# Performance work log

Hardware: AMD Instinct MI355X
Metric: run time of the kernel (lower is better)

## Reference

```python
import jax, jax.numpy as jnp
import numpy as np

B, S, D, R = 8, 512, 1024, 128

def setup_inputs() -> dict:
    key = jax.random.key(0)
    k1, k2 = jax.random.split(key)
    batch = jax.random.normal(k1, (B, S, D), dtype=jnp.float32)
    # nn.init.uniform_(proj, -0.05, 0.05)
    proj = jax.random.uniform(k2, (D, R), dtype=jnp.float32, minval=-0.05, maxval=0.05)
    return {"batch": batch, "proj": proj}

def reference(batch, proj):
    # transformed: [B, S, R]
    transformed = jnp.matmul(batch, proj)
    # pairwise squared distances via broadcast diff (same math as expand/transpose/diff/pow/sum)
    diffs = transformed[:, :, None, :] - transformed[:, None, :, :]  # [B, S, S, R]
    squared_distances = jnp.sum(diffs * diffs, axis=-1)              # [B, S, S]
    return squared_distances
```

## Files before the change

### kernel.cpp

```cpp
#include <hip/hip_runtime.h>
#include <hip/hip_bf16.h>

constexpr int B_ = 8;
constexpr int S_ = 512;
constexpr int D_ = 1024;
constexpr int R_ = 128;
constexpr int M_ = B_ * S_;

typedef unsigned short u16;
typedef __attribute__((ext_vector_type(8))) short short8;
typedef __attribute__((ext_vector_type(4))) float f32x4;

static __device__ __forceinline__ u16 f2bf(float f) {
    unsigned u = __float_as_uint(f);
    u += 0x7fffu + ((u >> 16) & 1u);
    return (u16)(u >> 16);
}
static __device__ __forceinline__ float bf2f(u16 u) {
    return __uint_as_float((unsigned)u << 16);
}

__global__ __launch_bounds__(256) void transpose_proj_kernel(
    const float* __restrict__ P, u16* __restrict__ Pt)
{
    __shared__ float S[16][132];
    const int t  = threadIdx.x;
    const int kk = blockIdx.x;
    const int kq = blockIdx.y;

#pragma unroll
    for (int p = 0; p < 2; ++p) {
        const int k = (t >> 5) + p * 8;
        const int c = (t & 31) * 4;
        *reinterpret_cast<float4*>(&S[k][c]) =
            *reinterpret_cast<const float4*>(
                &P[(size_t)(kk * 64 + kq * 16 + k) * R_ + c]);
    }
    __syncthreads();

    const int col = t >> 1;
    const int h   = t & 1;
    unsigned u[4];
#pragma unroll
    for (int q = 0; q < 4; ++q) {
        const u16 lo = f2bf(S[h * 8 + q * 2 + 0][col]);
        const u16 hi = f2bf(S[h * 8 + q * 2 + 1][col]);
        u[q] = (unsigned)lo | ((unsigned)hi << 16);
    }
    *reinterpret_cast<uint4*>(&Pt[(size_t)kk * 8192 + col * 64 + kq * 16 + h * 8]) =
        make_uint4(u[0], u[1], u[2], u[3]);
}

__global__ __launch_bounds__(256) void gemm1_kernel(
    const float* __restrict__ A,
    const u16* __restrict__ Pt,
    u16* __restrict__ T)
{
    __shared__ u16 As[2][16][72];
    __shared__ u16 Bs[2][64][72];

    const int t    = threadIdx.x;
    const int row0 = blockIdx.y * 16;
    const int col0 = blockIdx.x * 64;
    const int w    = t >> 6;
    const int l    = t & 63;
    const int g    = l >> 4;
    const int l15  = l & 15;

    f32x4 acc = f32x4{0.f, 0.f, 0.f, 0.f};

    const int ar = t >> 4;
    const int aq = t & 15;
    const int bcol = t >> 2;
    const int bq   = t & 3;

    const float* Abase = &A[(size_t)(row0 + ar) * D_ + aq * 4];

    float4 areg[16];
#pragma unroll
    for (int kk = 0; kk < 16; ++kk)
        areg[kk] = *reinterpret_cast<const float4*>(Abase + kk * 64);

    const uint4* b0src = reinterpret_cast<const uint4*>(
        &Pt[(size_t)0 * 8192 + (col0 + bcol) * 64 + bq * 16]);
    uint4 bp0 = b0src[0];
    uint4 bp1 = b0src[1];

#pragma unroll
    for (int kk = 0; kk < 16; ++kk) {
        const int cur = kk & 1;
        {
            const float4 v = areg[kk];
            const u16 c0 = f2bf(v.x), c1 = f2bf(v.y), c2 = f2bf(v.z), c3 = f2bf(v.w);
            const unsigned lo = (unsigned)c0 | ((unsigned)c1 << 16);
            const unsigned hi = (unsigned)c2 | ((unsigned)c3 << 16);
            *reinterpret_cast<uint2*>(&As[cur][ar][aq * 4]) = make_uint2(lo, hi);
            uint4* bdst = reinterpret_cast<uint4*>(&Bs[cur][bcol][bq * 16]);
            bdst[0] = bp0;
            bdst[1] = bp1;
        }
        if (kk + 1 < 16) {
            const uint4* bs = reinterpret_cast<const uint4*>(
                &Pt[(size_t)(kk + 1) * 8192 + (col0 + bcol) * 64 + bq * 16]);
            bp0 = bs[0];
            bp1 = bs[1];
        }
        __syncthreads();

#pragma unroll
        for (int h2 = 0; h2 < 2; ++h2) {
            const short8 a = *reinterpret_cast<const short8*>(
                &As[cur][l15][h2 * 32 + g * 8]);
            const short8 b = *reinterpret_cast<const short8*>(
                &Bs[cur][w * 16 + l15][h2 * 32 + g * 8]);
            acc = __builtin_amdgcn_mfma_f32_16x16x32_bf16(a, b, acc, 0, 0, 0);
        }
    }

#pragma unroll
    for (int r = 0; r < 4; ++r) {
        const int row = row0 + g * 4 + r;
        const int col = col0 + w * 16 + l15;
        T[(size_t)row * R_ + col] = f2bf(acc[r]);
    }
}

__global__ __launch_bounds__(256) void pairdist_kernel(
    const u16* __restrict__ T,
    float* __restrict__ out)
{
    __shared__ u16 Ti[64][136];
    __shared__ u16 Tj[64][136];
    __shared__ float ni[64], nj[64];

    const int t  = threadIdx.x;
    const int b  = blockIdx.z;
    const int i0 = blockIdx.y * 64;
    const int j0 = blockIdx.x * 64;
    const u16* Tb = T + (size_t)b * S_ * R_;

    const int w   = t >> 6;
    const int l   = t & 63;
    const int g   = l >> 4;
    const int l15 = l & 15;

    {
        const int r  = t >> 2;
        const int kq = (t & 3) * 32;
        const uint4* si = reinterpret_cast<const uint4*>(&Tb[(size_t)(i0 + r) * R_ + kq]);
        const uint4* sj = reinterpret_cast<const uint4*>(&Tb[(size_t)(j0 + r) * R_ + kq]);
        uint4* di = reinterpret_cast<uint4*>(&Ti[r][kq]);
        uint4* dj = reinterpret_cast<uint4*>(&Tj[r][kq]);
#pragma unroll
        for (int p = 0; p < 4; ++p) { di[p] = si[p]; dj[p] = sj[p]; }
    }
    __syncthreads();

    if (t < 128) {
        const u16* rowp = (t < 64) ? &Ti[t][0] : &Tj[t - 64][0];
        float s = 0.f;
#pragma unroll
        for (int p = 0; p < 16; ++p) {
            const uint4 v = *reinterpret_cast<const uint4*>(rowp + p * 8);
            const unsigned uu[4] = {v.x, v.y, v.z, v.w};
#pragma unroll
            for (int q = 0; q < 4; ++q) {
                const float f0 = bf2f((u16)(uu[q] & 0xffffu));
                const float f1 = bf2f((u16)(uu[q] >> 16));
                s += f0 * f0 + f1 * f1;
            }
        }
        if (t < 64) ni[t] = s; else nj[t - 64] = s;
    }
    __syncthreads();

    f32x4 acc[4];
#pragma unroll
    for (int n = 0; n < 4; ++n) acc[n] = f32x4{0.f, 0.f, 0.f, 0.f};

#pragma unroll
    for (int kk = 0; kk < 4; ++kk) {
        const short8 a = *reinterpret_cast<const short8*>(
            &Ti[w * 16 + l15][kk * 32 + g * 8]);
#pragma unroll
        for (int n = 0; n < 4; ++n) {
            const short8 bb = *reinterpret_cast<const short8*>(
                &Tj[n * 16 + l15][kk * 32 + g * 8]);
            acc[n] = __builtin_amdgcn_mfma_f32_16x16x32_bf16(a, bb, acc[n], 0, 0, 0);
        }
    }

    float niv[4];
#pragma unroll
    for (int r = 0; r < 4; ++r) niv[r] = ni[w * 16 + g * 4 + r];
#pragma unroll
    for (int n = 0; n < 4; ++n) {
        const float njv = nj[n * 16 + l15];
#pragma unroll
        for (int r = 0; r < 4; ++r) {
            const int row = i0 + w * 16 + g * 4 + r;
            const int col = j0 + n * 16 + l15;
            out[((size_t)b * S_ + row) * S_ + col] = niv[r] + njv - 2.f * acc[n][r];
        }
    }
}

extern "C" void kernel_launch(void* const* d_in, const int* in_sizes, int n_in,
                              void* d_out, int out_size, void* d_ws, size_t ws_size,
                              hipStream_t stream) {
    const float* batch = (const float*)d_in[0];
    const float* proj  = (const float*)d_in[1];
    float* out = (float*)d_out;

    u16* Pt = (u16*)d_ws;
    u16* T  = Pt + 16 * 8192;

    transpose_proj_kernel<<<dim3(16, 4), 256, 0, stream>>>(proj, Pt);
    gemm1_kernel<<<dim3(2, M_ / 16), 256, 0, stream>>>(batch, Pt, T);
    pairdist_kernel<<<dim3(S_ / 64, S_ / 64, B_), 256, 0, stream>>>(T, out);
}
```

Measured before the change: 78.73 us.

## Fuse three kernels into one cooperative kernel with grid syncs

Merges the proj transpose, the projection GEMM and the pairwise-distance kernel into a single cooperative launch of 512 blocks. Grid-wide barriers replace kernel boundaries, and shared memory is reused across the three phases. This aims to remove two kernel-launch gaps, at the cost of grid.sync overhead and a fixed grid size that must be fully co-resident.

```diff
diff --git a/kernel.cpp b/kernel.cpp
--- a/kernel.cpp
+++ b/kernel.cpp
@@ -1,5 +1,8 @@
 #include <hip/hip_runtime.h>
 #include <hip/hip_bf16.h>
+#include <hip/hip_cooperative_groups.h>
+
+namespace cg = cooperative_groups;
 
 constexpr int B_ = 8;
 constexpr int S_ = 512;
@@ -20,187 +23,199 @@
     return __uint_as_float((unsigned)u << 16);
 }
 
-__global__ __launch_bounds__(256) void transpose_proj_kernel(
-    const float* __restrict__ P, u16* __restrict__ Pt)
-{
-    __shared__ float S[16][132];
-    const int t  = threadIdx.x;
-    const int kk = blockIdx.x;
-    const int kq = blockIdx.y;
-
-#pragma unroll
-    for (int p = 0; p < 2; ++p) {
-        const int k = (t >> 5) + p * 8;
-        const int c = (t & 31) * 4;
-        *reinterpret_cast<float4*>(&S[k][c]) =
-            *reinterpret_cast<const float4*>(
-                &P[(size_t)(kk * 64 + kq * 16 + k) * R_ + c]);
-    }
-    __syncthreads();
-
-    const int col = t >> 1;
-    const int h   = t & 1;
-    unsigned u[4];
-#pragma unroll
-    for (int q = 0; q < 4; ++q) {
-        const u16 lo = f2bf(S[h * 8 + q * 2 + 0][col]);
-        const u16 hi = f2bf(S[h * 8 + q * 2 + 1][col]);
-        u[q] = (unsigned)lo | ((unsigned)hi << 16);
-    }
-    *reinterpret_cast<uint4*>(&Pt[(size_t)kk * 8192 + col * 64 + kq * 16 + h * 8]) =
-        make_uint4(u[0], u[1], u[2], u[3]);
-}
-
-__global__ __launch_bounds__(256) void gemm1_kernel(
-    const float* __restrict__ A,
-    const u16* __restrict__ Pt,
-    u16* __restrict__ T)
-{
-    __shared__ u16 As[2][16][72];
-    __shared__ u16 Bs[2][64][72];
-
-    const int t    = threadIdx.x;
-    const int row0 = blockIdx.y * 16;
-    const int col0 = blockIdx.x * 64;
-    const int w    = t >> 6;
-    const int l    = t & 63;
-    const int g    = l >> 4;
-    const int l15  = l & 15;
-
-    f32x4 acc = f32x4{0.f, 0.f, 0.f, 0.f};
-
-    const int ar = t >> 4;
-    const int aq = t & 15;
-    const int bcol = t >> 2;
-    const int bq   = t & 3;
-
-    const float* Abase = &A[(size_t)(row0 + ar) * D_ + aq * 4];
-
-    float4 areg[16];
-#pragma unroll
-    for (int kk = 0; kk < 16; ++kk)
-        areg[kk] = *reinterpret_cast<const float4*>(Abase + kk * 64);
-
-    const uint4* b0src = reinterpret_cast<const uint4*>(
-        &Pt[(size_t)0 * 8192 + (col0 + bcol) * 64 + bq * 16]);
-    uint4 bp0 = b0src[0];
-    uint4 bp1 = b0src[1];
-
-#pragma unroll
-    for (int kk = 0; kk < 16; ++kk) {
-        const int cur = kk & 1;
-        {
-            const float4 v = areg[kk];
-            const u16 c0 = f2bf(v.x), c1 = f2bf(v.y), c2 = f2bf(v.z), c3 = f2bf(v.w);
-            const unsigned lo = (unsigned)c0 | ((unsigned)c1 << 16);
-            const unsigned hi = (unsigned)c2 | ((unsigned)c3 << 16);
-            *reinterpret_cast<uint2*>(&As[cur][ar][aq * 4]) = make_uint2(lo, hi);
-            uint4* bdst = reinterpret_cast<uint4*>(&Bs[cur][bcol][bq * 16]);
-            bdst[0] = bp0;
-            bdst[1] = bp1;
-        }
-        if (kk + 1 < 16) {
-            const uint4* bs = reinterpret_cast<const uint4*>(
-                &Pt[(size_t)(kk + 1) * 8192 + (col0 + bcol) * 64 + bq * 16]);
-            bp0 = bs[0];
-            bp1 = bs[1];
-        }
-        __syncthreads();
-
-#pragma unroll
-        for (int h2 = 0; h2 < 2; ++h2) {
-            const short8 a = *reinterpret_cast<const short8*>(
-                &As[cur][l15][h2 * 32 + g * 8]);
-            const short8 b = *reinterpret_cast<const short8*>(
-                &Bs[cur][w * 16 + l15][h2 * 32 + g * 8]);
-            acc = __builtin_amdgcn_mfma_f32_16x16x32_bf16(a, b, acc, 0, 0, 0);
-        }
-    }
-
-#pragma unroll
-    for (int r = 0; r < 4; ++r) {
-        const int row = row0 + g * 4 + r;
-        const int col = col0 + w * 16 + l15;
-        T[(size_t)row * R_ + col] = f2bf(acc[r]);
-    }
-}
-
-__global__ __launch_bounds__(256) void pairdist_kernel(
-    const u16* __restrict__ T,
+__global__ __launch_bounds__(256) void fused_kernel(
+    const float* __restrict__ batch,
+    const float* __restrict__ proj,
+    u16* __restrict__ Pt,
+    u16* __restrict__ T,
     float* __restrict__ out)
 {
-    __shared__ u16 Ti[64][136];
-    __shared__ u16 Tj[64][136];
-    __shared__ float ni[64], nj[64];
-
-    const int t  = threadIdx.x;
-    const int b  = blockIdx.z;
-    const int i0 = blockIdx.y * 64;
-    const int j0 = blockIdx.x * 64;
-    const u16* Tb = T + (size_t)b * S_ * R_;
+    __shared__ __align__(16) char smem[35328];
+
+    const int bid = blockIdx.x;
+    const int t   = threadIdx.x;
+    cg::grid_group grid = cg::this_grid();
 
     const int w   = t >> 6;
     const int l   = t & 63;
     const int g   = l >> 4;
     const int l15 = l & 15;
 
+    if (bid < 64) {
+        float (*S)[132] = reinterpret_cast<float(*)[132]>(smem);
+        const int kk = bid >> 2;
+        const int kq = bid & 3;
+
+#pragma unroll
+        for (int p = 0; p < 2; ++p) {
+            const int k = (t >> 5) + p * 8;
+            const int c = (t & 31) * 4;
+            *reinterpret_cast<float4*>(&S[k][c]) =
+                *reinterpret_cast<const float4*>(
+                    &proj[(size_t)(kk * 64 + kq * 16 + k) * R_ + c]);
+        }
+        __syncthreads();
+
+        const int col = t >> 1;
+        const int h   = t & 1;
+        unsigned u[4];
+#pragma unroll
+        for (int q = 0; q < 4; ++q) {
+            const u16 lo = f2bf(S[h * 8 + q * 2 + 0][col]);
+            const u16 hi = f2bf(S[h * 8 + q * 2 + 1][col]);
+            u[q] = (unsigned)lo | ((unsigned)hi << 16);
+        }
+        *reinterpret_cast<uint4*>(
+            &Pt[(size_t)kk * 8192 + col * 64 + kq * 16 + h * 8]) =
+            make_uint4(u[0], u[1], u[2], u[3]);
+    }
+    __threadfence();
+    grid.sync();
+
     {
-        const int r  = t >> 2;
-        const int kq = (t & 3) * 32;
-        const uint4* si = reinterpret_cast<const uint4*>(&Tb[(size_t)(i0 + r) * R_ + kq]);
-        const uint4* sj = reinterpret_cast<const uint4*>(&Tb[(size_t)(j0 + r) * R_ + kq]);
-        uint4* di = reinterpret_cast<uint4*>(&Ti[r][kq]);
-        uint4* dj = reinterpret_cast<uint4*>(&Tj[r][kq]);
-#pragma unroll
-        for (int p = 0; p < 4; ++p) { di[p] = si[p]; dj[p] = sj[p]; }
+        typedef u16 AsT[2][16][72];
+        typedef u16 BsT[2][64][72];
+        AsT& As = *reinterpret_cast<AsT*>(smem);
+        BsT& Bs = *reinterpret_cast<BsT*>(smem + 4608);
+
+        const int row0 = (bid >> 1) * 16;
+        const int col0 = (bid & 1) * 64;
+
+        f32x4 acc = f32x4{0.f, 0.f, 0.f, 0.f};
+
+        const int ar = t >> 4;
+        const int aq = t & 15;
+        const int bcol = t >> 2;
+        const int bq   = t & 3;
+
+        const float* Abase = &batch[(size_t)(row0 + ar) * D_ + aq * 4];
+
+        float4 areg[16];
+#pragma unroll
+        for (int kk = 0; kk < 16; ++kk)
+            areg[kk] = *reinterpret_cast<const float4*>(Abase + kk * 64);
+
+        const uint4* b0src = reinterpret_cast<const uint4*>(
+            &Pt[(size_t)0 * 8192 + (col0 + bcol) * 64 + bq * 16]);
+        uint4 bp0 = b0src[0];
+        uint4 bp1 = b0src[1];
+
+#pragma unroll
+        for (int kk = 0; kk < 16; ++kk) {
+            const int cur = kk & 1;
+            {
+                const float4 v = areg[kk];
+                const u16 c0 = f2bf(v.x), c1 = f2bf(v.y),
+                          c2 = f2bf(v.z), c3 = f2bf(v.w);
+                const unsigned lo = (unsigned)c0 | ((unsigned)c1 << 16);
+                const unsigned hi = (unsigned)c2 | ((unsigned)c3 << 16);
+                *reinterpret_cast<uint2*>(&As[cur][ar][aq * 4]) = make_uint2(lo, hi);
+                uint4* bdst = reinterpret_cast<uint4*>(&Bs[cur][bcol][bq * 16]);
+                bdst[0] = bp0;
+                bdst[1] = bp1;
+            }
+            if (kk + 1 < 16) {
+                const uint4* bs = reinterpret_cast<const uint4*>(
+                    &Pt[(size_t)(kk + 1) * 8192 + (col0 + bcol) * 64 + bq * 16]);
+                bp0 = bs[0];
+                bp1 = bs[1];
+            }
+            __syncthreads();
+
+#pragma unroll
+            for (int h2 = 0; h2 < 2; ++h2) {
+                const short8 a = *reinterpret_cast<const short8*>(
+                    &As[cur][l15][h2 * 32 + g * 8]);
+                const short8 b = *reinterpret_cast<const short8*>(
+                    &Bs[cur][w * 16 + l15][h2 * 32 + g * 8]);
+                acc = __builtin_amdgcn_mfma_f32_16x16x32_bf16(a, b, acc, 0, 0, 0);
+            }
+        }
+
+#pragma unroll
+        for (int r = 0; r < 4; ++r) {
+            const int row = row0 + g * 4 + r;
+            const int col = col0 + w * 16 + l15;
+            T[(size_t)row * R_ + col] = f2bf(acc[r]);
+        }
     }
-    __syncthreads();
-
-    if (t < 128) {
-        const u16* rowp = (t < 64) ? &Ti[t][0] : &Tj[t - 64][0];
-        float s = 0.f;
-#pragma unroll
-        for (int p = 0; p < 16; ++p) {
-            const uint4 v = *reinterpret_cast<const uint4*>(rowp + p * 8);
-            const unsigned uu[4] = {v.x, v.y, v.z, v.w};
-#pragma unroll
-            for (int q = 0; q < 4; ++q) {
-                const float f0 = bf2f((u16)(uu[q] & 0xffffu));
-                const float f1 = bf2f((u16)(uu[q] >> 16));
-                s += f0 * f0 + f1 * f1;
-            }
-        }
-        if (t < 64) ni[t] = s; else nj[t - 64] = s;
-    }
-    __syncthreads();
-
-    f32x4 acc[4];
-#pragma unroll
-    for (int n = 0; n < 4; ++n) acc[n] = f32x4{0.f, 0.f, 0.f, 0.f};
-
-#pragma unroll
-    for (int kk = 0; kk < 4; ++kk) {
-        const short8 a = *reinterpret_cast<const short8*>(
-            &Ti[w * 16 + l15][kk * 32 + g * 8]);
+    __threadfence();
+    grid.sync();
+
+    {
+        typedef u16 PanelT[64][136];
+        PanelT& Ti = *reinterpret_cast<PanelT*>(smem);
+        PanelT& Tj = *reinterpret_cast<PanelT*>(smem + 17408);
+        float* ni = reinterpret_cast<float*>(smem + 34816);
+        float* nj = reinterpret_cast<float*>(smem + 35072);
+
+        const int jb = bid & 7;
+        const int ib = (bid >> 3) & 7;
+        const int b  = bid >> 6;
+        const int i0 = ib * 64;
+        const int j0 = jb * 64;
+        const u16* Tb = T + (size_t)b * S_ * R_;
+
+        {
+            const int r  = t >> 2;
+            const int kq = (t & 3) * 32;
+            const uint4* si = reinterpret_cast<const uint4*>(
+                &Tb[(size_t)(i0 + r) * R_ + kq]);
+            const uint4* sj = reinterpret_cast<const uint4*>(
+                &Tb[(size_t)(j0 + r) * R_ + kq]);
+            uint4* di = reinterpret_cast<uint4*>(&Ti[r][kq]);
+            uint4* dj = reinterpret_cast<uint4*>(&Tj[r][kq]);
+#pragma unroll
+            for (int p = 0; p < 4; ++p) { di[p] = si[p]; dj[p] = sj[p]; }
+        }
+        __syncthreads();
+
+        if (t < 128) {
+            const u16* rowp = (t < 64) ? &Ti[t][0] : &Tj[t - 64][0];
+            float s = 0.f;
+#pragma unroll
+            for (int p = 0; p < 16; ++p) {
+                const uint4 v = *reinterpret_cast<const uint4*>(rowp + p * 8);
+                const unsigned uu[4] = {v.x, v.y, v.z, v.w};
+#pragma unroll
+                for (int q = 0; q < 4; ++q) {
+                    const float f0 = bf2f((u16)(uu[q] & 0xffffu));
+                    const float f1 = bf2f((u16)(uu[q] >> 16));
+                    s += f0 * f0 + f1 * f1;
+                }
+            }
+            if (t < 64) ni[t] = s; else nj[t - 64] = s;
+        }
+        __syncthreads();
+
+        f32x4 acc[4];
+#pragma unroll
+        for (int n = 0; n < 4; ++n) acc[n] = f32x4{0.f, 0.f, 0.f, 0.f};
+
+#pragma unroll
+        for (int kk = 0; kk < 4; ++kk) {
+            const short8 a = *reinterpret_cast<const short8*>(
+                &Ti[w * 16 + l15][kk * 32 + g * 8]);
+#pragma unroll
+            for (int n = 0; n < 4; ++n) {
+                const short8 bb = *reinterpret_cast<const short8*>(
+                    &Tj[n * 16 + l15][kk * 32 + g * 8]);
+                acc[n] = __builtin_amdgcn_mfma_f32_16x16x32_bf16(a, bb, acc[n], 0, 0, 0);
+            }
+        }
+
+        float niv[4];
+#pragma unroll
+        for (int r = 0; r < 4; ++r) niv[r] = ni[w * 16 + g * 4 + r];
 #pragma unroll
         for (int n = 0; n < 4; ++n) {
-            const short8 bb = *reinterpret_cast<const short8*>(
-                &Tj[n * 16 + l15][kk * 32 + g * 8]);
-            acc[n] = __builtin_amdgcn_mfma_f32_16x16x32_bf16(a, bb, acc[n], 0, 0, 0);
-        }
-    }
-
-    float niv[4];
-#pragma unroll
-    for (int r = 0; r < 4; ++r) niv[r] = ni[w * 16 + g * 4 + r];
-#pragma unroll
-    for (int n = 0; n < 4; ++n) {
-        const float njv = nj[n * 16 + l15];
-#pragma unroll
-        for (int r = 0; r < 4; ++r) {
-            const int row = i0 + w * 16 + g * 4 + r;
-            const int col = j0 + n * 16 + l15;
-            out[((size_t)b * S_ + row) * S_ + col] = niv[r] + njv - 2.f * acc[n][r];
+            const float njv = nj[n * 16 + l15];
+#pragma unroll
+            for (int r = 0; r < 4; ++r) {
+                const int row = i0 + w * 16 + g * 4 + r;
+                const int col = j0 + n * 16 + l15;
+                out[((size_t)b * S_ + row) * S_ + col] = niv[r] + njv - 2.f * acc[n][r];
+            }
         }
     }
 }
@@ -215,7 +230,7 @@
     u16* Pt = (u16*)d_ws;
     u16* T  = Pt + 16 * 8192;
 
-    transpose_proj_kernel<<<dim3(16, 4), 256, 0, stream>>>(proj, Pt);
-    gemm1_kernel<<<dim3(2, M_ / 16), 256, 0, stream>>>(batch, Pt, T);
-    pairdist_kernel<<<dim3(S_ / 64, S_ / 64, B_), 256, 0, stream>>>(T, out);
-}
+    void* args[] = {(void*)&batch, (void*)&proj, (void*)&Pt, (void*)&T, (void*)&out};
+    hipLaunchCooperativeKernel((const void*)fused_kernel,
+                               dim3(512), dim3(256), args, 0, stream);
+}
```

Result: slower. 294.0 us (+273.5%).
